# Kernel optimization log

Hardware: AMD Instinct MI355X
Metric: run time of the kernel (lower is better)

Reference implementation:

```python
import jax, jax.numpy as jnp
import numpy as np

N, E, S, K, NB = 16384, 262144, 10, 64, 8
R_MAX, P_CUT, AVG_NEIGH = 5.0, 5, 16.0
L_OF_LM = np.array([0, 1, 1, 1, 2, 2, 2, 2, 2])  # l value of each of the 9 lm components
L_SLICES = [(0, 1), (1, 4), (4, 9)]               # lm ranges for l = 0,1,2
MLP_H = 16


def _sph(u):
    # real spherical harmonics up to l=2, e3nn 'component' normalization (sum_m Y_lm^2 = 2l+1)
    x, y, z = u[..., 0], u[..., 1], u[..., 2]
    s3, s15, s5 = np.float32(np.sqrt(3.0)), np.float32(np.sqrt(15.0)), np.float32(np.sqrt(5.0))
    return jnp.stack([
        jnp.ones_like(x),
        s3 * x, s3 * y, s3 * z,
        s15 * x * y, s15 * y * z, (s5 / 2) * (3 * z * z - 1), s15 * x * z, (s15 / 2) * (x * x - y * y),
    ], axis=-1)


def _radial(r):
    # Bessel radial basis with smooth polynomial cutoff envelope (p = P_CUT)
    u = r / R_MAX
    r_safe = jnp.where(r > 1e-9, r, 1.0)
    n = jnp.arange(1, NB + 1, dtype=r.dtype)
    bess = np.float32(np.sqrt(2.0 / R_MAX)) * jnp.sin(n * jnp.pi * u[:, None]) / r_safe[:, None]
    p = float(P_CUT)
    env = 1.0 - (p + 1) * (p + 2) / 2 * u**P_CUT + p * (p + 2) * u**(P_CUT + 1) - p * (p + 1) / 2 * u**(P_CUT + 2)
    env = jnp.where(u < 1.0, env, 0.0)
    return bess * env[:, None]  # [E, NB]


def setup_inputs() -> dict:
    key = jax.random.key(0)
    ks = jax.random.split(key, 16)
    positions = jax.random.uniform(ks[0], (N, 3), jnp.float32) * 4.0  # box so many edges fall inside r_max
    species = jax.random.randint(ks[1], (N,), 0, S)
    senders = jax.random.randint(ks[2], (E,), 0, N)
    receivers = jax.random.randint(ks[3], (E,), 0, N)
    shifts = jnp.zeros((E, 3), jnp.float32)
    W_embed = jax.random.normal(ks[4], (S, K), jnp.float32)
    W_rad = jax.random.normal(ks[5], (2, 3, NB, K), jnp.float32) * 0.3
    W_mix = jax.random.normal(ks[6], (2, 3, K, K), jnp.float32) / np.sqrt(K)
    W_prod = jax.random.normal(ks[7], (2, 3, 3, K), jnp.float32) * 0.1
    W_sc = jax.random.normal(ks[8], (2, S, 3, K, K), jnp.float32) / np.sqrt(K)
    W_ro0 = jax.random.normal(ks[9], (K,), jnp.float32) / np.sqrt(K)
    W_m1 = jax.random.normal(ks[10], (K, MLP_H), jnp.float32) / np.sqrt(K)
    b_m1 = jnp.zeros((MLP_H,), jnp.float32)
    W_m2 = jax.random.normal(ks[11], (MLP_H,), jnp.float32) / np.sqrt(MLP_H)
    return dict(positions=positions, shifts=shifts, species=species, senders=senders,
                receivers=receivers, W_embed=W_embed, W_rad=W_rad, W_mix=W_mix,
                W_prod=W_prod, W_sc=W_sc, W_ro0=W_ro0, W_m1=W_m1, b_m1=b_m1, W_m2=W_m2)


def reference(positions, shifts, species, senders, receivers, W_embed, W_rad, W_mix,
              W_prod, W_sc, W_ro0, W_m1, b_m1, W_m2):
    lm = jnp.asarray(L_OF_LM)
    onehot = jax.nn.one_hot(species, S, dtype=positions.dtype)
    # node embedding: scalars only -> feats [N, 9(lm), K]
    feats = jnp.zeros((N, 9, K), positions.dtype).at[:, 0, :].set(onehot @ W_embed)

    # edge geometry
    vec = positions[receivers] - positions[senders] + shifts           # [E, 3]
    r = jnp.linalg.norm(vec, axis=-1)                                  # [E]
    u_hat = vec / jnp.where(r > 1e-9, r, 1.0)[:, None]
    Y = _sph(u_hat)                                                     # [E, 9]
    rad = _radial(r)                                                    # [E, NB]

    energies = []
    for i in range(2):
        # interaction: radial-weighted SH messages from sender scalars, scatter-sum to receivers
        hs = feats[:, 0, :][senders]                                    # [E, K]
        Rl = jnp.einsum('eb,lbk->elk', rad, W_rad[i])[:, lm, :]         # [E, 9, K]
        msg = hs[:, None, :] * Y[:, :, None] * Rl                       # [E, 9, K]
        A = jax.ops.segment_sum(msg, receivers, num_segments=N) / AVG_NEIGH
        A = jnp.einsum('nmk,mkj->nmj', A, W_mix[i][lm])                 # per-l channel mixing

        # correlation-3 equivariant product basis (symmetric-contraction style)
        A0 = A[:, 0, :]
        inv = jnp.sum(A * A, axis=1)                                    # rotation-invariant [N, K]
        w1, w2, w3 = (W_prod[i, j][lm] for j in range(3))               # each [9, K]
        B = A * (w1[None] + w2[None] * A0[:, None, :] + w3[None] * inv[:, None, :])

        # species-dependent self-connection (linear of feats x node_attrs), per-l weights
        sc = jnp.concatenate([
            jnp.einsum('nmk,ns,skj->nmj', feats[:, st:en], onehot, W_sc[i, :, l])
            for l, (st, en) in enumerate(L_SLICES)], axis=1)
        feats = B + sc

        if i == 0:
            energies.append(feats[:, 0, :] @ W_ro0)                     # linear readout
        else:
            feats = feats.at[:, 1:, :].set(0.0)                         # last layer keeps 0e only
            energies.append(jax.nn.silu(feats[:, 0, :] @ W_m1 + b_m1) @ W_m2)

    return jnp.stack(energies, axis=1)  # [N, num_interactions]
```

## Files before the change

kernel.cpp:

```cpp
#include <hip/hip_runtime.h>

#define NN 16384
#define NE 262144
#define NSPEC 10
#define KC 64
#define MLPH 16
#define SEG 128
#define EPSG 2048

__device__ __forceinline__ float wave_reduce(float v) {
#pragma unroll
    for (int off = 32; off > 0; off >>= 1) v += __shfl_down(v, off, 64);
    return v;
}

__device__ __forceinline__ float f4c(const float4& v, int j) {
    const float* p = &v.x;
    return p[j];
}

__global__ void __launch_bounds__(1024) k_pre(
    const float* __restrict__ W_embed,
    const int* __restrict__ species,
    const int* __restrict__ receivers,
    int* __restrict__ eslot,
    unsigned short* __restrict__ cnt16,
    float4* __restrict__ h04) {
    __shared__ int cntL[NN];
    int t = threadIdx.x;
#pragma unroll
    for (int i = 0; i < 16; ++i) cntL[t + 1024 * i] = 0;
    __syncthreads();
    int ebase = blockIdx.x * EPSG;
#pragma unroll
    for (int j = 0; j < EPSG / 1024; ++j) {
        int e = ebase + j * 1024 + t;
        int r = receivers[e];
        eslot[e] = atomicAdd(&cntL[r], 1);
    }
    int gt = blockIdx.x * 1024 + t;
#pragma unroll
    for (int q = 0; q < 2; ++q) {
        int idx = gt * 2 + q;
        int n = idx >> 4, w = idx & 15;
        h04[idx] = reinterpret_cast<const float4*>(W_embed + species[n] * KC)[w];
    }
    __syncthreads();
    unsigned short* o = cnt16 + (size_t)blockIdx.x * NN;
#pragma unroll
    for (int i = 0; i < 16; ++i)
        o[t + 1024 * i] = (unsigned short)cntL[t + 1024 * i];
}

__global__ void __launch_bounds__(128) k_colscan(
    const unsigned short* __restrict__ cnt16,
    int* __restrict__ seg_base,
    int* __restrict__ count) {
    int r = blockIdx.x * 128 + threadIdx.x;
    int run = 0;
#pragma unroll 4
    for (int g = 0; g < SEG; ++g) {
        int c = cnt16[(size_t)g * NN + r];
        seg_base[(size_t)g * NN + r] = run;
        run += c;
    }
    count[r] = run;
}

__global__ void __launch_bounds__(1024) k_scan(
    const int* __restrict__ count, int* __restrict__ row_start,
    const int* __restrict__ species, int* __restrict__ nslot,
    int* __restrict__ sp_start) {
    __shared__ int lds[1024];
    __shared__ int itercnt[256 * NSPEC];
    __shared__ int spt[NSPEC];
    int t = threadIdx.x;
    int lane = t & 63;
    int w = t >> 6;
#pragma unroll
    for (int j = 0; j < 16; ++j) {
        int n = w * 1024 + j * 64 + lane;
        int sp = species[n];
#pragma unroll
        for (int s = 0; s < NSPEC; ++s) {
            unsigned long long mask = __ballot(sp == s);
            if (lane == 0) itercnt[(w * 16 + j) * NSPEC + s] = (int)__popcll(mask);
        }
    }
    int base = t * 16;
    int local[16];
    int ssum = 0;
#pragma unroll
    for (int b = 0; b < 16; ++b) { local[b] = count[base + b]; ssum += local[b]; }
    lds[t] = ssum;
    __syncthreads();
    for (int off = 1; off < 1024; off <<= 1) {
        int v = (t >= off) ? lds[t - off] : 0;
        __syncthreads();
        lds[t] += v;
        __syncthreads();
    }
    int run = lds[t] - ssum;
#pragma unroll
    for (int b = 0; b < 16; ++b) { row_start[base + b] = run; run += local[b]; }
    if (t == 1023) row_start[NN] = run;
    __syncthreads();
    if (t < NSPEC) {
        int r2 = 0;
        for (int i = 0; i < 256; ++i) {
            int v = itercnt[i * NSPEC + t];
            itercnt[i * NSPEC + t] = r2;
            r2 += v;
        }
        spt[t] = r2;
    }
    __syncthreads();
    if (t == 0) {
        int r2 = 0;
        for (int s = 0; s < NSPEC; ++s) { sp_start[s] = r2; r2 += spt[s]; }
        sp_start[NSPEC] = r2;
    }
#pragma unroll
    for (int j = 0; j < 16; ++j) {
        int n = w * 1024 + j * 64 + lane;
        int sp = species[n];
        int rank = 0;
#pragma unroll
        for (int s = 0; s < NSPEC; ++s) {
            unsigned long long mask = __ballot(sp == s);
            if (sp == s)
                rank = (int)__popcll(mask & ((1ull << lane) - 1ull));
        }
        nslot[n] = itercnt[(w * 16 + j) * NSPEC + sp] + rank;
    }
}

__global__ void k_geom(const float* __restrict__ pos,
                       const float* __restrict__ shifts,
                       const int* __restrict__ senders,
                       const int* __restrict__ receivers,
                       const int* __restrict__ row_start,
                       const int* __restrict__ seg_base,
                       const int* __restrict__ eslot,
                       const int* __restrict__ species,
                       const int* __restrict__ sp_start,
                       const int* __restrict__ nslot,
                       int* __restrict__ ord,
                       float* __restrict__ edgerec) {
    int e = blockIdx.x * 256 + threadIdx.x;
    if (e < NN) {
        int sp = species[e];
        ord[sp_start[sp] + nslot[e]] = e;
    }
    int s = senders[e], r = receivers[e];
    float dx = pos[r * 3 + 0] - pos[s * 3 + 0] + shifts[e * 3 + 0];
    float dy = pos[r * 3 + 1] - pos[s * 3 + 1] + shifts[e * 3 + 1];
    float dz = pos[r * 3 + 2] - pos[s * 3 + 2] + shifts[e * 3 + 2];
    float rn = sqrtf(dx * dx + dy * dy + dz * dz);
    float den = (rn > 1e-9f) ? rn : 1.0f;
    float x = dx / den, y = dy / den, z = dz / den;
    const float s3  = 1.7320508075688772f;
    const float s15 = 3.8729833462074170f;
    const float s5h = 1.1180339887498949f;
    const float s15h = 1.9364916731037085f;
    float rec[20];
    rec[0] = 1.0f;
    rec[1] = s3 * x;
    rec[2] = s3 * y;
    rec[3] = s3 * z;
    rec[4] = s15 * x * y;
    rec[5] = s15 * y * z;
    rec[6] = s5h * (3.0f * z * z - 1.0f);
    rec[7] = s15 * x * z;
    rec[8] = s15h * (x * x - y * y);
    float u = rn * 0.2f;
    float env = 0.0f;
    if (u < 1.0f) {
        float u2 = u * u;
        float u5 = u2 * u2 * u;
        env = 1.0f - 21.0f * u5 + 35.0f * u5 * u - 15.0f * u5 * u2;
    }
    float pre = 0.63245553203367587f * env / den;
#pragma unroll
    for (int nb = 1; nb <= 8; ++nb)
        rec[8 + nb] = pre * sinf((float)nb * 3.14159265358979323846f * u);
    rec[17] = __int_as_float(s);
    rec[18] = 0.f; rec[19] = 0.f;
    int p = row_start[r] + seg_base[(size_t)(e >> 11) * NN + r] + eslot[e];
    float4* o = (float4*)(edgerec + (size_t)p * 20);
#pragma unroll
    for (int i = 0; i < 5; ++i)
        o[i] = make_float4(rec[4 * i], rec[4 * i + 1], rec[4 * i + 2], rec[4 * i + 3]);
}

__device__ __forceinline__ void agg_edge(const float* __restrict__ rec, float hv,
                                         const float (&Wr)[3][8], float (&acc)[9]) {
    float R0 = 0.f, R1 = 0.f, R2 = 0.f;
#pragma unroll
    for (int b = 0; b < 8; ++b) {
        float rb = rec[9 + b];
        R0 += rb * Wr[0][b];
        R1 += rb * Wr[1][b];
        R2 += rb * Wr[2][b];
    }
    float t0 = hv * R0, t1 = hv * R1, t2 = hv * R2;
    acc[0] += t0 * rec[0];
    acc[1] += t1 * rec[1];
    acc[2] += t1 * rec[2];
    acc[3] += t1 * rec[3];
    acc[4] += t2 * rec[4];
    acc[5] += t2 * rec[5];
    acc[6] += t2 * rec[6];
    acc[7] += t2 * rec[7];
    acc[8] += t2 * rec[8];
}

#define AMX_NPW 4
__global__ void __launch_bounds__(512) k_aggmix(
    const float* __restrict__ h,
    const float* __restrict__ edgerec,
    const int* __restrict__ row_start,
    const float* __restrict__ Wr_i,
    const float* __restrict__ Wm_i,
    const float* __restrict__ Wp_i,
    float* __restrict__ Bm0) {
    __shared__ float Wlds[3 * 4096];
    __shared__ float xtile[8][9 * 64];
    {
        float4* Wl4 = (float4*)Wlds;
        const float4* W4 = (const float4*)Wm_i;
#pragma unroll
        for (int i = 0; i < 6; ++i)
            Wl4[threadIdx.x + 512 * i] = W4[threadIdx.x + 512 * i];
    }
    __syncthreads();
    int lane = threadIdx.x & 63;
    int wid = __builtin_amdgcn_readfirstlane(threadIdx.x >> 6);
    float* xt = xtile[wid];
    float Wr[3][8];
#pragma unroll
    for (int l = 0; l < 3; ++l)
#pragma unroll
        for (int b = 0; b < 8; ++b) Wr[l][b] = Wr_i[(l * 8 + b) * 64 + lane];
    float w10 = Wp_i[0 * 64 + lane];
    float w20 = Wp_i[3 * 64 + lane];
    float w30 = Wp_i[6 * 64 + lane];
    int n0 = (blockIdx.x * 8 + wid) * AMX_NPW;
    for (int it = 0; it < AMX_NPW; ++it) {
        int n = n0 + it;
        float acc[9];
#pragma unroll
        for (int m = 0; m < 9; ++m) acc[m] = 0.f;
        int e0 = row_start[n], e1 = row_start[n + 1];
        int e = e0;
        for (; e + 2 <= e1; e += 2) {
            const float* ra = edgerec + (size_t)e * 20;
            const float* rb = ra + 20;
            int sa = __float_as_int(ra[17]);
            int sb = __float_as_int(rb[17]);
            float ha = h[(size_t)sa * 64 + lane];
            float hb = h[(size_t)sb * 64 + lane];
            agg_edge(ra, ha, Wr, acc);
            agg_edge(rb, hb, Wr, acc);
        }
        if (e < e1) {
            const float* ra = edgerec + (size_t)e * 20;
            int sa = __float_as_int(ra[17]);
            float ha = h[(size_t)sa * 64 + lane];
            agg_edge(ra, ha, Wr, acc);
        }
        const float inv_avg = 1.0f / 16.0f;
#pragma unroll
        for (int m = 0; m < 9; ++m) xt[m * 64 + lane] = acc[m] * inv_avg;
        float mix[9];
#pragma unroll
        for (int m = 0; m < 9; ++m) mix[m] = 0.f;
#pragma unroll 2
        for (int c4 = 0; c4 < 16; ++c4) {
            float4 xb[9];
#pragma unroll
            for (int m = 0; m < 9; ++m)
                xb[m] = *(const float4*)&xt[m * 64 + c4 * 4];
#pragma unroll
            for (int j = 0; j < 4; ++j) {
                int k = c4 * 4 + j;
                float wv0 = Wlds[k * 64 + lane];
                float wv1 = Wlds[4096 + k * 64 + lane];
                float wv2 = Wlds[8192 + k * 64 + lane];
                mix[0] += f4c(xb[0], j) * wv0;
                mix[1] += f4c(xb[1], j) * wv1;
                mix[2] += f4c(xb[2], j) * wv1;
                mix[3] += f4c(xb[3], j) * wv1;
                mix[4] += f4c(xb[4], j) * wv2;
                mix[5] += f4c(xb[5], j) * wv2;
                mix[6] += f4c(xb[6], j) * wv2;
                mix[7] += f4c(xb[7], j) * wv2;
                mix[8] += f4c(xb[8], j) * wv2;
            }
        }
        float A0 = mix[0];
        float inv = 0.f;
#pragma unroll
        for (int m = 0; m < 9; ++m) inv += mix[m] * mix[m];
        Bm0[(size_t)n * 64 + lane] = mix[0] * (w10 + w20 * A0 + w30 * inv);
    }
}

#define RPB 32
template <int ITER>
__global__ void __launch_bounds__(256) k_sc(
    const float* __restrict__ h_in,
    const float* __restrict__ Bm0,
    float* __restrict__ h_out,
    const int* __restrict__ ord,
    const int* __restrict__ sp_start,
    const float* __restrict__ Wsc_i,
    const float* __restrict__ W_ro0,
    const float* __restrict__ W_m1,
    const float* __restrict__ b_m1,
    const float* __restrict__ W_m2,
    float* __restrict__ out) {
    const int BPS = NN / RPB;
    int sp = blockIdx.x / BPS;
    int c  = blockIdx.x - sp * BPS;
    int base = sp_start[sp];
    int cnt  = sp_start[sp + 1] - base;
    int r0 = c * RPB;
    __shared__ float Wlds[4096];
    __shared__ float xtile[4][8 * 64];
    if (r0 < cnt) {
        const float4* W4 = (const float4*)(Wsc_i + (size_t)sp * 3 * 4096);
        float4* Wl4 = (float4*)Wlds;
#pragma unroll
        for (int i = 0; i < 4; ++i)
            Wl4[threadIdx.x + 256 * i] = W4[threadIdx.x + 256 * i];
    }
    __syncthreads();
    if (r0 >= cnt) return;
    int lane = threadIdx.x & 63;
    int wid = threadIdx.x >> 6;
    float* xt = xtile[wid];
    int rend = min(r0 + RPB, cnt);
    int q0 = r0 + wid * 8;
    if (q0 >= rend) return;
    int nd[8];
#pragma unroll
    for (int t = 0; t < 8; ++t)
        nd[t] = ord[base + min(q0 + t, rend - 1)];
    float xv[8];
#pragma unroll
    for (int t = 0; t < 8; ++t) xv[t] = h_in[(size_t)nd[t] * 64 + lane];
#pragma unroll
    for (int t = 0; t < 8; ++t) xt[t * 64 + lane] = xv[t];
    float acc[8];
#pragma unroll
    for (int t = 0; t < 8; ++t) acc[t] = 0.f;
#pragma unroll 2
    for (int c4 = 0; c4 < 16; ++c4) {
        float wv[4];
#pragma unroll
        for (int j = 0; j < 4; ++j) wv[j] = Wlds[(c4 * 4 + j) * 64 + lane];
#pragma unroll
        for (int t = 0; t < 8; ++t) {
            float4 xb = *(const float4*)&xt[t * 64 + c4 * 4];
#pragma unroll
            for (int j = 0; j < 4; ++j) acc[t] += f4c(xb, j) * wv[j];
        }
    }
    float wro = W_ro0[lane];
#pragma unroll
    for (int t = 0; t < 8; ++t) {
        if (q0 + t >= rend) break;
        int node = nd[t];
        float outv = acc[t] + Bm0[(size_t)node * 64 + lane];
        if (ITER == 0) {
            h_out[(size_t)node * 64 + lane] = outv;
            float e = wave_reduce(outv * wro);
            if (lane == 0) out[2 * node + 0] = e;
        } else {
            int hh = lane & 15;
            float tacc = b_m1[hh];
#pragma unroll
            for (int k = 0; k < 64; ++k)
                tacc += __shfl(outv, k, 64) * W_m1[k * MLPH + hh];
            float sig = 1.0f / (1.0f + expf(-tacc));
            float contrib = (lane < MLPH) ? tacc * sig * W_m2[lane] : 0.f;
            float e = wave_reduce(contrib);
            if (lane == 0) out[2 * node + 1] = e;
        }
    }
}

extern "C" void kernel_launch(void* const* d_in, const int* in_sizes, int n_in,
                              void* d_out, int out_size, void* d_ws, size_t ws_size,
                              hipStream_t stream) {
    const float* positions = (const float*)d_in[0];
    const float* shifts    = (const float*)d_in[1];
    const int*   species   = (const int*)d_in[2];
    const int*   senders   = (const int*)d_in[3];
    const int*   receivers = (const int*)d_in[4];
    const float* W_embed   = (const float*)d_in[5];
    const float* W_rad     = (const float*)d_in[6];
    const float* W_mix     = (const float*)d_in[7];
    const float* W_prod    = (const float*)d_in[8];
    const float* W_sc      = (const float*)d_in[9];
    const float* W_ro0     = (const float*)d_in[10];
    const float* W_m1      = (const float*)d_in[11];
    const float* b_m1      = (const float*)d_in[12];
    const float* W_m2      = (const float*)d_in[13];
    float* out = (float*)d_out;

    char* p = (char*)d_ws;
    float* edgerec = (float*)p; p += (size_t)NE * 20 * 4;
    int* seg_base  = (int*)p;   p += (size_t)SEG * NN * 4;
    float* Bm0     = (float*)p; p += (size_t)NN * KC * 4;
    float* h0      = (float*)p; p += (size_t)NN * KC * 4;
    float* h1      = (float*)p; p += (size_t)NN * KC * 4;
    unsigned short* cnt16 = (unsigned short*)p; p += (size_t)SEG * NN * 2;
    int* eslot     = (int*)p; p += (size_t)NE * 4;
    int* nslot     = (int*)p; p += (size_t)NN * 4;
    int* ord       = (int*)p; p += (size_t)NN * 4;
    int* count     = (int*)p; p += (size_t)NN * 4;
    int* row_start = (int*)p; p += (size_t)(NN + 1) * 4;
    int* sp_start  = (int*)p; p += 16 * 4;

    k_pre<<<SEG, 1024, 0, stream>>>(W_embed, species, receivers,
                                    eslot, cnt16, (float4*)h0);
    k_colscan<<<NN / 128, 128, 0, stream>>>(cnt16, seg_base, count);
    k_scan<<<1, 1024, 0, stream>>>(count, row_start, species, nslot, sp_start);
    k_geom<<<NE / 256, 256, 0, stream>>>(positions, shifts, senders, receivers,
                                         row_start, seg_base, eslot, species,
                                         sp_start, nslot, ord, edgerec);

    k_aggmix<<<NN / 32, 512, 0, stream>>>(h0, edgerec, row_start,
                                          W_rad + 0, W_mix + 0, W_prod + 0, Bm0);
    k_sc<0><<<NSPEC * (NN / RPB), 256, 0, stream>>>(h0, Bm0, h1, ord, sp_start,
        W_sc + 0, W_ro0, W_m1, b_m1, W_m2, out);

    k_aggmix<<<NN / 32, 512, 0, stream>>>(h1, edgerec, row_start,
                                          W_rad + 1536, W_mix + 12288,
                                          W_prod + 576, Bm0);
    k_sc<1><<<NSPEC * (NN / RPB), 256, 0, stream>>>(h1, Bm0, h0 , ord,
        sp_start, W_sc + (size_t)NSPEC * 3 * 4096, W_ro0, W_m1, b_m1, W_m2, out);
}
```

Measured before the change: 305.9 us.

## Compact edge records to 16 floats, split senders, transpose mix weights in LDS

Edge records drop the constant Y00 term and the embedded sender index, shrinking them from 20 to 16 floats, and senders move to a separate int array. The mix weights are stored transposed in LDS with a padded row stride of 65, so each lane reads float4 weight vectors instead of scalar loads. The 1/16 averaging factor is folded into the radial weights, and the edge loop becomes a single unrolled loop. The goal is less edge-record traffic and fewer LDS instructions in the mixing step. The costs are an extra gather from the sender array, possible misalignment of float4 LDS reads at the 65-float stride, and scattered stores when transposing the weights.

```diff
diff --git a/kernel.cpp b/kernel.cpp
--- a/kernel.cpp
+++ b/kernel.cpp
@@ -7,6 +7,7 @@
 #define MLPH 16
 #define SEG 128
 #define EPSG 2048
+#define WROW 65
 
 __device__ __forceinline__ float wave_reduce(float v) {
 #pragma unroll
@@ -146,7 +147,8 @@
                        const int* __restrict__ sp_start,
                        const int* __restrict__ nslot,
                        int* __restrict__ ord,
-                       float* __restrict__ edgerec) {
+                       float* __restrict__ edgerec,
+                       int* __restrict__ ssend) {
     int e = blockIdx.x * 256 + threadIdx.x;
     if (e < NN) {
         int sp = species[e];
@@ -163,16 +165,15 @@
     const float s15 = 3.8729833462074170f;
     const float s5h = 1.1180339887498949f;
     const float s15h = 1.9364916731037085f;
-    float rec[20];
-    rec[0] = 1.0f;
-    rec[1] = s3 * x;
-    rec[2] = s3 * y;
-    rec[3] = s3 * z;
-    rec[4] = s15 * x * y;
-    rec[5] = s15 * y * z;
-    rec[6] = s5h * (3.0f * z * z - 1.0f);
-    rec[7] = s15 * x * z;
-    rec[8] = s15h * (x * x - y * y);
+    float rec[16];
+    rec[0] = s3 * x;
+    rec[1] = s3 * y;
+    rec[2] = s3 * z;
+    rec[3] = s15 * x * y;
+    rec[4] = s15 * y * z;
+    rec[5] = s5h * (3.0f * z * z - 1.0f);
+    rec[6] = s15 * x * z;
+    rec[7] = s15h * (x * x - y * y);
     float u = rn * 0.2f;
     float env = 0.0f;
     if (u < 1.0f) {
@@ -183,14 +184,13 @@
     float pre = 0.63245553203367587f * env / den;
 #pragma unroll
     for (int nb = 1; nb <= 8; ++nb)
-        rec[8 + nb] = pre * sinf((float)nb * 3.14159265358979323846f * u);
-    rec[17] = __int_as_float(s);
-    rec[18] = 0.f; rec[19] = 0.f;
+        rec[7 + nb] = pre * sinf((float)nb * 3.14159265358979323846f * u);
     int p = row_start[r] + seg_base[(size_t)(e >> 11) * NN + r] + eslot[e];
-    float4* o = (float4*)(edgerec + (size_t)p * 20);
-#pragma unroll
-    for (int i = 0; i < 5; ++i)
+    float4* o = (float4*)(edgerec + (size_t)p * 16);
+#pragma unroll
+    for (int i = 0; i < 4; ++i)
         o[i] = make_float4(rec[4 * i], rec[4 * i + 1], rec[4 * i + 2], rec[4 * i + 3]);
+    ssend[p] = s;
 }
 
 __device__ __forceinline__ void agg_edge(const float* __restrict__ rec, float hv,
@@ -198,40 +198,51 @@
     float R0 = 0.f, R1 = 0.f, R2 = 0.f;
 #pragma unroll
     for (int b = 0; b < 8; ++b) {
-        float rb = rec[9 + b];
+        float rb = rec[8 + b];
         R0 += rb * Wr[0][b];
         R1 += rb * Wr[1][b];
         R2 += rb * Wr[2][b];
     }
     float t0 = hv * R0, t1 = hv * R1, t2 = hv * R2;
-    acc[0] += t0 * rec[0];
-    acc[1] += t1 * rec[1];
-    acc[2] += t1 * rec[2];
-    acc[3] += t1 * rec[3];
-    acc[4] += t2 * rec[4];
-    acc[5] += t2 * rec[5];
-    acc[6] += t2 * rec[6];
-    acc[7] += t2 * rec[7];
-    acc[8] += t2 * rec[8];
+    acc[0] += t0;
+    acc[1] += t1 * rec[0];
+    acc[2] += t1 * rec[1];
+    acc[3] += t1 * rec[2];
+    acc[4] += t2 * rec[3];
+    acc[5] += t2 * rec[4];
+    acc[6] += t2 * rec[5];
+    acc[7] += t2 * rec[6];
+    acc[8] += t2 * rec[7];
 }
 
 #define AMX_NPW 4
 __global__ void __launch_bounds__(512) k_aggmix(
     const float* __restrict__ h,
     const float* __restrict__ edgerec,
+    const int* __restrict__ ssend,
     const int* __restrict__ row_start,
     const float* __restrict__ Wr_i,
     const float* __restrict__ Wm_i,
     const float* __restrict__ Wp_i,
     float* __restrict__ Bm0) {
-    __shared__ float Wlds[3 * 4096];
+    __shared__ float Wlds[3 * 64 * WROW];
     __shared__ float xtile[8][9 * 64];
     {
-        float4* Wl4 = (float4*)Wlds;
         const float4* W4 = (const float4*)Wm_i;
 #pragma unroll
-        for (int i = 0; i < 6; ++i)
-            Wl4[threadIdx.x + 512 * i] = W4[threadIdx.x + 512 * i];
+        for (int i = 0; i < 6; ++i) {
+            int idx4 = i * 512 + threadIdx.x;
+            float4 v = W4[idx4];
+            int l = idx4 >> 10;
+            int rem = idx4 & 1023;
+            int k = rem >> 4;
+            int c0 = (rem & 15) * 4;
+            float* dst = Wlds + l * 64 * WROW + k;
+            dst[(c0 + 0) * WROW] = v.x;
+            dst[(c0 + 1) * WROW] = v.y;
+            dst[(c0 + 2) * WROW] = v.z;
+            dst[(c0 + 3) * WROW] = v.w;
+        }
     }
     __syncthreads();
     int lane = threadIdx.x & 63;
@@ -241,10 +252,14 @@
 #pragma unroll
     for (int l = 0; l < 3; ++l)
 #pragma unroll
-        for (int b = 0; b < 8; ++b) Wr[l][b] = Wr_i[(l * 8 + b) * 64 + lane];
+        for (int b = 0; b < 8; ++b)
+            Wr[l][b] = Wr_i[(l * 8 + b) * 64 + lane] * (1.0f / 16.0f);
     float w10 = Wp_i[0 * 64 + lane];
     float w20 = Wp_i[3 * 64 + lane];
     float w30 = Wp_i[6 * 64 + lane];
+    const float* Wt0 = Wlds + (size_t)lane * WROW;
+    const float* Wt1 = Wlds + 64 * WROW + (size_t)lane * WROW;
+    const float* Wt2 = Wlds + 128 * WROW + (size_t)lane * WROW;
     int n0 = (blockIdx.x * 8 + wid) * AMX_NPW;
     for (int it = 0; it < AMX_NPW; ++it) {
         int n = n0 + it;
@@ -252,50 +267,38 @@
 #pragma unroll
         for (int m = 0; m < 9; ++m) acc[m] = 0.f;
         int e0 = row_start[n], e1 = row_start[n + 1];
-        int e = e0;
-        for (; e + 2 <= e1; e += 2) {
-            const float* ra = edgerec + (size_t)e * 20;
-            const float* rb = ra + 20;
-            int sa = __float_as_int(ra[17]);
-            int sb = __float_as_int(rb[17]);
-            float ha = h[(size_t)sa * 64 + lane];
-            float hb = h[(size_t)sb * 64 + lane];
-            agg_edge(ra, ha, Wr, acc);
-            agg_edge(rb, hb, Wr, acc);
-        }
-        if (e < e1) {
-            const float* ra = edgerec + (size_t)e * 20;
-            int sa = __float_as_int(ra[17]);
-            float ha = h[(size_t)sa * 64 + lane];
-            agg_edge(ra, ha, Wr, acc);
-        }
-        const float inv_avg = 1.0f / 16.0f;
-#pragma unroll
-        for (int m = 0; m < 9; ++m) xt[m * 64 + lane] = acc[m] * inv_avg;
+#pragma unroll 4
+        for (int e = e0; e < e1; ++e) {
+            int s = ssend[e];
+            float hv = h[(size_t)s * 64 + lane];
+            const float* rc = edgerec + (size_t)e * 16;
+            agg_edge(rc, hv, Wr, acc);
+        }
+#pragma unroll
+        for (int m = 0; m < 9; ++m) xt[m * 64 + lane] = acc[m];
         float mix[9];
 #pragma unroll
         for (int m = 0; m < 9; ++m) mix[m] = 0.f;
-#pragma unroll 2
+#pragma unroll 4
         for (int c4 = 0; c4 < 16; ++c4) {
+            float4 wv0 = *(const float4*)&Wt0[c4 * 4];
+            float4 wv1 = *(const float4*)&Wt1[c4 * 4];
+            float4 wv2 = *(const float4*)&Wt2[c4 * 4];
             float4 xb[9];
 #pragma unroll
             for (int m = 0; m < 9; ++m)
                 xb[m] = *(const float4*)&xt[m * 64 + c4 * 4];
 #pragma unroll
             for (int j = 0; j < 4; ++j) {
-                int k = c4 * 4 + j;
-                float wv0 = Wlds[k * 64 + lane];
-                float wv1 = Wlds[4096 + k * 64 + lane];
-                float wv2 = Wlds[8192 + k * 64 + lane];
-                mix[0] += f4c(xb[0], j) * wv0;
-                mix[1] += f4c(xb[1], j) * wv1;
-                mix[2] += f4c(xb[2], j) * wv1;
-                mix[3] += f4c(xb[3], j) * wv1;
-                mix[4] += f4c(xb[4], j) * wv2;
-                mix[5] += f4c(xb[5], j) * wv2;
-                mix[6] += f4c(xb[6], j) * wv2;
-                mix[7] += f4c(xb[7], j) * wv2;
-                mix[8] += f4c(xb[8], j) * wv2;
+                mix[0] += f4c(xb[0], j) * f4c(wv0, j);
+                mix[1] += f4c(xb[1], j) * f4c(wv1, j);
+                mix[2] += f4c(xb[2], j) * f4c(wv1, j);
+                mix[3] += f4c(xb[3], j) * f4c(wv1, j);
+                mix[4] += f4c(xb[4], j) * f4c(wv2, j);
+                mix[5] += f4c(xb[5], j) * f4c(wv2, j);
+                mix[6] += f4c(xb[6], j) * f4c(wv2, j);
+                mix[7] += f4c(xb[7], j) * f4c(wv2, j);
+                mix[8] += f4c(xb[8], j) * f4c(wv2, j);
             }
         }
         float A0 = mix[0];
@@ -411,13 +414,14 @@
     float* out = (float*)d_out;
 
     char* p = (char*)d_ws;
-    float* edgerec = (float*)p; p += (size_t)NE * 20 * 4;
+    float* edgerec = (float*)p; p += (size_t)NE * 16 * 4;
     int* seg_base  = (int*)p;   p += (size_t)SEG * NN * 4;
     float* Bm0     = (float*)p; p += (size_t)NN * KC * 4;
     float* h0      = (float*)p; p += (size_t)NN * KC * 4;
     float* h1      = (float*)p; p += (size_t)NN * KC * 4;
     unsigned short* cnt16 = (unsigned short*)p; p += (size_t)SEG * NN * 2;
     int* eslot     = (int*)p; p += (size_t)NE * 4;
+    int* ssend     = (int*)p; p += (size_t)NE * 4;
     int* nslot     = (int*)p; p += (size_t)NN * 4;
     int* ord       = (int*)p; p += (size_t)NN * 4;
     int* count     = (int*)p; p += (size_t)NN * 4;
@@ -430,14 +434,14 @@
     k_scan<<<1, 1024, 0, stream>>>(count, row_start, species, nslot, sp_start);
     k_geom<<<NE / 256, 256, 0, stream>>>(positions, shifts, senders, receivers,
                                          row_start, seg_base, eslot, species,
-                                         sp_start, nslot, ord, edgerec);
-
-    k_aggmix<<<NN / 32, 512, 0, stream>>>(h0, edgerec, row_start,
+                                         sp_start, nslot, ord, edgerec, ssend);
+
+    k_aggmix<<<NN / 32, 512, 0, stream>>>(h0, edgerec, ssend, row_start,
                                           W_rad + 0, W_mix + 0, W_prod + 0, Bm0);
     k_sc<0><<<NSPEC * (NN / RPB), 256, 0, stream>>>(h0, Bm0, h1, ord, sp_start,
         W_sc + 0, W_ro0, W_m1, b_m1, W_m2, out);
 
-    k_aggmix<<<NN / 32, 512, 0, stream>>>(h1, edgerec, row_start,
+    k_aggmix<<<NN / 32, 512, 0, stream>>>(h1, edgerec, ssend, row_start,
                                           W_rad + 1536, W_mix + 12288,
                                           W_prod + 576, Bm0);
     k_sc<1><<<NSPEC * (NN / RPB), 256, 0, stream>>>(h1, Bm0, h0 , ord,
```

Result: slower. 415.1 us (+35.7%).
